# Kernel tuning notes

Hardware: AMD Instinct MI355X
Metric: run time of the kernel (lower is better)

The kernel has to match this reference:

```python
import jax, jax.numpy as jnp
import numpy as np

N_NODES = 100000
N_EDGES = 1600000
IN_CH, HID, OUT = 128, 64, 32


def gcn_conv(x, W, b, src, dst, n_nodes):
    """PyG-style GCNConv: add self-loops, sym-normalize, linear, aggregate."""
    h = x @ W  # [N, out] transform first (cheaper than transforming messages)
    loops = jnp.arange(n_nodes, dtype=src.dtype)
    s = jnp.concatenate([src, loops])
    d = jnp.concatenate([dst, loops])
    deg = jax.ops.segment_sum(jnp.ones_like(d, dtype=h.dtype), d, num_segments=n_nodes)
    dinv = jnp.where(deg > 0, jax.lax.rsqrt(deg), 0.0)
    norm = dinv[s] * dinv[d]  # [E+N]
    msg = h[s] * norm[:, None]  # gather + scale
    out = jax.ops.segment_sum(msg, d, num_segments=n_nodes)  # scatter-add
    return out + b


def setup_inputs() -> dict:
    key = jax.random.key(0)
    ks = jax.random.split(key, 8)
    x = jax.random.normal(ks[0], (N_NODES, IN_CH), dtype=jnp.float32)
    edge_index = jax.random.randint(ks[1], (2, N_EDGES), 0, N_NODES, dtype=jnp.int64)
    # Glorot-ish init for weights
    W1 = jax.random.normal(ks[2], (IN_CH, HID), dtype=jnp.float32) * (1.0 / np.sqrt(IN_CH))
    b1 = jnp.zeros((HID,), dtype=jnp.float32)
    W_mu = jax.random.normal(ks[3], (HID, OUT), dtype=jnp.float32) * (1.0 / np.sqrt(HID))
    b_mu = jnp.zeros((OUT,), dtype=jnp.float32)
    W_ls = jax.random.normal(ks[4], (HID, OUT), dtype=jnp.float32) * (1.0 / np.sqrt(HID))
    b_ls = jnp.zeros((OUT,), dtype=jnp.float32)
    return {"x": x, "edge_index": edge_index, "W1": W1, "b1": b1,
            "W_mu": W_mu, "b_mu": b_mu, "W_ls": W_ls, "b_ls": b_ls}


def reference(x, edge_index, W1, b1, W_mu, b_mu, W_ls, b_ls):
    src, dst = edge_index[0], edge_index[1]
    h = jax.nn.relu(gcn_conv(x, W1, b1, src, dst, N_NODES))
    # dropout: eval-mode identity
    mu = gcn_conv(h, W_mu, b_mu, src, dst, N_NODES)
    logstd = gcn_conv(h, W_ls, b_ls, src, dst, N_NODES)
    return (mu, logstd)
```

## Files before the change

kernel.cpp:

```cpp
#include <hip/hip_runtime.h>
#include <hip/hip_fp16.h>

#define NN 100000
#define NE 1600000
#define BKT_STRIDE 64
#define GRP 224
#define NB 447
#define SCAP 4096
#define ACHUNK 6400
#define ABLK (NE / ACHUNK)

typedef int      v2i  __attribute__((ext_vector_type(2)));
typedef int      v4i  __attribute__((ext_vector_type(4)));
typedef float    v4f  __attribute__((ext_vector_type(4)));
typedef _Float16 f16x4 __attribute__((ext_vector_type(4)));
typedef _Float16 f16x8 __attribute__((ext_vector_type(8)));
typedef float    f32x4 __attribute__((ext_vector_type(4)));

union frag_u { f16x8 v8; f16x4 v4[2]; };

__global__ __launch_bounds__(256) void k_part(const int* __restrict__ src, const int* __restrict__ dst,
                                              int* __restrict__ wc, int* __restrict__ pairs) {
  __shared__ int cntb[512];
  __shared__ int scanb[512];
  __shared__ int ofs[512];
  __shared__ int gbase[512];
  __shared__ v2i stg[ACHUNK];
  int tid = threadIdx.x;
  int e0 = blockIdx.x * ACHUNK;
  cntb[tid] = 0; cntb[tid + 256] = 0;
  __syncthreads();
  for (int k = tid; k < ACHUNK; k += 256) {
    int d = __builtin_nontemporal_load(dst + e0 + k);
    atomicAdd(&cntb[d / GRP], 1);
  }
  __syncthreads();
  scanb[tid] = cntb[tid]; scanb[tid + 256] = cntb[tid + 256];
  __syncthreads();
  for (int off = 1; off < 512; off <<= 1) {
    int a0 = (tid >= off) ? scanb[tid - off] : 0;
    int a1 = scanb[tid + 256 - off];
    __syncthreads();
    scanb[tid] += a0; scanb[tid + 256] += a1;
    __syncthreads();
  }
  ofs[tid] = scanb[tid] - cntb[tid];
  ofs[tid + 256] = scanb[tid + 256] - cntb[tid + 256];
  if (tid < NB && cntb[tid]) gbase[tid] = atomicAdd(&wc[tid], cntb[tid]);
  if (tid + 256 < NB && cntb[tid + 256]) gbase[tid + 256] = atomicAdd(&wc[tid + 256], cntb[tid + 256]);
  __syncthreads();
  for (int k = tid; k < ACHUNK; k += 256) {
    int d = __builtin_nontemporal_load(dst + e0 + k);
    int s = __builtin_nontemporal_load(src + e0 + k);
    int g = d / GRP;
    int p = atomicAdd(&ofs[g], 1);
    v2i sd; sd.x = s; sd.y = d;
    stg[p] = sd;
  }
  __syncthreads();
  for (int i = tid; i < ACHUNK; i += 256) {
    v2i sd = stg[i];
    int g = sd.y / GRP;
    int excl = scanb[g] - cntb[g];
    int o = gbase[g] + (i - excl);
    if (o < SCAP)
      pairs[(size_t)g * SCAP + o] = sd.x | ((sd.y - g * GRP) << 17);
  }
}

__global__ __launch_bounds__(256) void k_bktbuild(const int* __restrict__ pairs, const int* __restrict__ wc,
                                                  int* __restrict__ cnt, float* __restrict__ dinv,
                                                  int* __restrict__ bkt) {
  __shared__ int lb[GRP * BKT_STRIDE];
  __shared__ int lc[GRP];
  int tid = threadIdx.x;
  int g = blockIdx.x;
  int base = g * GRP;
  int nvalid = (NN - base < GRP) ? (NN - base) : GRP;
  {
    v4i sent; sent.x = NN; sent.y = NN; sent.z = NN; sent.w = NN;
    v4i* lb4 = (v4i*)lb;
#pragma unroll
    for (int i = 0; i < (GRP * BKT_STRIDE / 4) / 256; ++i) lb4[tid + 256 * i] = sent;
  }
  if (tid < GRP) lc[tid] = 0;
  __syncthreads();
  int n = wc[g];
  if (n > SCAP) n = SCAP;
  const int* seg = pairs + (size_t)g * SCAP;
  for (int i = tid; i < n; i += 256) {
    int p = seg[i];
    int s = p & 0x1FFFF;
    int dl = p >> 17;
    int pos = atomicAdd(&lc[dl], 1);
    if (pos < BKT_STRIDE) lb[dl * BKT_STRIDE + pos] = s;
  }
  __syncthreads();
  int tot4 = nvalid * BKT_STRIDE / 4;
  v4i* out4 = (v4i*)(bkt + (size_t)base * BKT_STRIDE);
  const v4i* lb4 = (const v4i*)lb;
  for (int i = tid; i < tot4; i += 256) out4[i] = lb4[i];
  if (tid < nvalid) {
    int c = lc[tid];
    if (c > BKT_STRIDE) c = BKT_STRIDE;
    cnt[base + tid] = c;
    dinv[base + tid] = rsqrtf((float)(c + 1));
  }
  if (g == 0 && tid == 0) dinv[NN] = 0.f;
}

__global__ __launch_bounds__(256) void k_gemm1(const float* __restrict__ x, const float* __restrict__ W,
                                               const float* __restrict__ dinv, __half* __restrict__ out) {
  __shared__ _Float16 Xs[64][136];
  __shared__ _Float16 Wt[64][136];
  int tid = threadIdx.x;
  int row0 = blockIdx.x * 64;
  {
    int c = tid & 63;
    int k0 = tid >> 6;
#pragma unroll
    for (int i = 0; i < 32; ++i) {
      int k = k0 + 4 * i;
      Wt[c][k] = (_Float16)W[k * 64 + c];
    }
  }
  {
#pragma unroll
    for (int i = 0; i < 8; ++i) {
      int idx = tid + 256 * i;
      int r = idx >> 5;
      int k4 = idx & 31;
      v4f v = {0.f, 0.f, 0.f, 0.f};
      if (row0 + r < NN)
        v = __builtin_nontemporal_load((const v4f*)(x + (size_t)(row0 + r) * 128 + k4 * 4));
      f16x4 h;
      h[0] = (_Float16)v.x; h[1] = (_Float16)v.y; h[2] = (_Float16)v.z; h[3] = (_Float16)v.w;
      *(f16x4*)&Xs[r][k4 * 4] = h;
    }
  }
  __syncthreads();
  int lane = tid & 63;
  int wv = tid >> 6;
  int l15 = lane & 15;
  int lq = lane >> 4;
  int rl = wv * 16 + l15;
  f32x4 acc[4] = {};
#pragma unroll
  for (int ks = 0; ks < 4; ++ks) {
    int ka = ks * 32 + lq * 4;
    frag_u bf;
    bf.v4[0] = *(const f16x4*)&Xs[rl][ka];
    bf.v4[1] = *(const f16x4*)&Xs[rl][ka + 16];
#pragma unroll
    for (int ct = 0; ct < 4; ++ct) {
      frag_u af;
      af.v4[0] = *(const f16x4*)&Wt[ct * 16 + l15][ka];
      af.v4[1] = *(const f16x4*)&Wt[ct * 16 + l15][ka + 16];
      acc[ct] = __builtin_amdgcn_mfma_f32_16x16x32_f16(af.v8, bf.v8, acc[ct], 0, 0, 0);
    }
  }
  int row = row0 + rl;
  if (row < NN) {
    float dr = dinv[row];
#pragma unroll
    for (int ct = 0; ct < 4; ++ct) {
      int c = ct * 16 + lq * 4;
      __half2 h01 = __floats2half2_rn(acc[ct][0] * dr, acc[ct][1] * dr);
      __half2 h23 = __floats2half2_rn(acc[ct][2] * dr, acc[ct][3] * dr);
      __half2* op = (__half2*)(out + (size_t)row * 64 + c);
      op[0] = h01;
      op[1] = h23;
    }
  }
}

template <bool PASS1>
__global__ __launch_bounds__(256) void k_agg(const __half* __restrict__ hin, const int* __restrict__ bkt,
                                             const int* __restrict__ cnt, const float* __restrict__ dinv,
                                             const float* __restrict__ bias, __half* __restrict__ outp) {
  int tid = threadIdx.x;
  int lane = tid & 63;
  int wv = tid >> 6;
  int node = blockIdx.x * 16 + wv * 4 + (lane >> 4);
  int ch0 = (lane & 15) * 4;
  float di = dinv[node];
  float a0, a1, a2, a3;
  {
    v2i raw = *(const v2i*)(hin + (size_t)node * 64 + ch0);
    float2 f01 = __half22float2(((const __half2*)&raw)[0]);
    float2 f23 = __half22float2(((const __half2*)&raw)[1]);
    a0 = f01.x; a1 = f01.y; a2 = f23.x; a3 = f23.y;
  }
  int n = (cnt[node] + 3) & ~3;
  const v4i* bp = (const v4i*)(bkt + node * BKT_STRIDE);
  for (int j = 0; j < n; j += 4, ++bp) {
    v4i b = *bp;
#pragma unroll
    for (int t = 0; t < 4; ++t) {
      int idx = (t == 0) ? b.x : (t == 1) ? b.y : (t == 2) ? b.z : b.w;
      v2i raw = *(const v2i*)(hin + (size_t)idx * 64 + ch0);
      float2 f01 = __half22float2(((const __half2*)&raw)[0]);
      float2 f23 = __half22float2(((const __half2*)&raw)[1]);
      a0 += f01.x; a1 += f01.y; a2 += f23.x; a3 += f23.y;
    }
  }
  float r0, r1, r2, r3;
  if (PASS1) {
    float4 bv = *(const float4*)(bias + ch0);
    r0 = di * fmaxf(di * a0 + bv.x, 0.f);
    r1 = di * fmaxf(di * a1 + bv.y, 0.f);
    r2 = di * fmaxf(di * a2 + bv.z, 0.f);
    r3 = di * fmaxf(di * a3 + bv.w, 0.f);
  } else {
    r0 = di * a0; r1 = di * a1; r2 = di * a2; r3 = di * a3;
  }
  __half2* op = (__half2*)(outp + (size_t)node * 64 + ch0);
  op[0] = __floats2half2_rn(r0, r1);
  op[1] = __floats2half2_rn(r2, r3);
}

__global__ __launch_bounds__(256) void k_gemm2(const __half* __restrict__ a, const float* __restrict__ Wmu,
                                               const float* __restrict__ Wls, const float* __restrict__ bmu,
                                               const float* __restrict__ bls, float* __restrict__ out) {
  __shared__ _Float16 Xs[64][72];
  __shared__ _Float16 Wt[64][72];
  int tid = threadIdx.x;
  int row0 = blockIdx.x * 64;
  {
    int c = tid & 63;
    int k0 = tid >> 6;
    const float* Wsrc = (c < 32) ? (Wmu + c) : (Wls + (c - 32));
#pragma unroll
    for (int i = 0; i < 16; ++i) {
      int k = k0 + 4 * i;
      Wt[c][k] = (_Float16)Wsrc[k * 32];
    }
  }
  {
#pragma unroll
    for (int i = 0; i < 2; ++i) {
      int idx = tid + 256 * i;
      int r = idx >> 3;
      int h8 = idx & 7;
      v4i raw = {0, 0, 0, 0};
      if (row0 + r < NN)
        raw = *(const v4i*)(a + (size_t)(row0 + r) * 64 + h8 * 8);
      *(v4i*)&Xs[r][h8 * 8] = raw;
    }
  }
  __syncthreads();
  int lane = tid & 63;
  int wv = tid >> 6;
  int l15 = lane & 15;
  int lq = lane >> 4;
  int rl = wv * 16 + l15;
  f32x4 acc[4] = {};
#pragma unroll
  for (int ks = 0; ks < 2; ++ks) {
    int ka = ks * 32 + lq * 4;
    frag_u bf;
    bf.v4[0] = *(const f16x4*)&Xs[rl][ka];
    bf.v4[1] = *(const f16x4*)&Xs[rl][ka + 16];
#pragma unroll
    for (int ct = 0; ct < 4; ++ct) {
      frag_u af;
      af.v4[0] = *(const f16x4*)&Wt[ct * 16 + l15][ka];
      af.v4[1] = *(const f16x4*)&Wt[ct * 16 + l15][ka + 16];
      acc[ct] = __builtin_amdgcn_mfma_f32_16x16x32_f16(af.v8, bf.v8, acc[ct], 0, 0, 0);
    }
  }
  int row = row0 + rl;
  if (row < NN) {
#pragma unroll
    for (int ct = 0; ct < 4; ++ct) {
      int c = ct * 16 + lq * 4;
      const float* bsrc = (c < 32) ? (bmu + c) : (bls + (c - 32));
      float4 o = make_float4(acc[ct][0] + bsrc[0], acc[ct][1] + bsrc[1],
                             acc[ct][2] + bsrc[2], acc[ct][3] + bsrc[3]);
      float* dst = (c < 32) ? (out + (size_t)row * 32 + c)
                            : (out + (size_t)NN * 32 + (size_t)row * 32 + (c - 32));
      *(float4*)dst = o;
    }
  }
}

extern "C" void kernel_launch(void* const* d_in, const int* in_sizes, int n_in,
                              void* d_out, int out_size, void* d_ws, size_t ws_size,
                              hipStream_t stream) {
  const float* x   = (const float*)d_in[0];
  const int*   ei  = (const int*)d_in[1];
  const float* W1  = (const float*)d_in[2];
  const float* b1  = (const float*)d_in[3];
  const float* Wmu = (const float*)d_in[4];
  const float* bmu = (const float*)d_in[5];
  const float* Wls = (const float*)d_in[6];
  const float* bls = (const float*)d_in[7];
  float* out = (float*)d_out;

  char* ws = (char*)d_ws;
  size_t off = 0;
  auto take = [&](size_t bytes) -> char* {
    char* p = ws + off;
    off = (off + bytes + 255) & ~(size_t)255;
    return p;
  };
  int*    cnt  = (int*)take((size_t)NN * 4);
  float*  dinv = (float*)take((size_t)(NN + 1) * 4);
  int*    bkt  = (int*)take((size_t)NN * BKT_STRIDE * 4);
  __half* hpre = (__half*)take((size_t)(NN + 1) * 64 * 2);
  __half* h1   = (__half*)take((size_t)(NN + 1) * 64 * 2);
  __half* agg2 = (__half*)take((size_t)(NN + 1) * 64 * 2);
  int*    wc   = (int*)take((size_t)512 * 4);

  int* pairs = (int*)hpre;

  const int* srcp = ei;
  const int* dstp = ei + NE;

  hipMemsetAsync(wc, 0, (size_t)512 * 4, stream);
  k_part<<<ABLK, 256, 0, stream>>>(srcp, dstp, wc, pairs);
  k_bktbuild<<<NB, 256, 0, stream>>>(pairs, wc, cnt, dinv, bkt);
  hipMemsetAsync(hpre + (size_t)NN * 64, 0, 64 * 2, stream);
  hipMemsetAsync(h1 + (size_t)NN * 64, 0, 64 * 2, stream);
  k_gemm1<<<(NN + 63) / 64, 256, 0, stream>>>(x, W1, dinv, hpre);
  k_agg<true><<<NN / 16, 256, 0, stream>>>(hpre, bkt, cnt, dinv, b1, h1);
  k_agg<false><<<NN / 16, 256, 0, stream>>>(h1, bkt, cnt, dinv, nullptr, agg2);
  k_gemm2<<<(NN + 63) / 64, 256, 0, stream>>>(agg2, Wmu, Wls, bmu, bls, out);
}
```

Baseline: 237.8 us.

## Fuse second aggregation into output GEMM and fold sentinel memsets into bucket build

The second neighbor aggregation now happens inside the final GEMM kernel. Each block gathers and sums rows for its 64 nodes and writes the normalized fp16 result straight into shared memory before the MFMA step. This removes the agg2 intermediate buffer's global write and read, plus one kernel launch. The two sentinel-row memsets are also folded into the bucket-build kernel. In exchange, the fused kernel runs with far fewer blocks (64 nodes per block, 4 passes per wave), which may lower memory-level parallelism for the latency-bound gathers.

```diff
diff --git a/kernel.cpp b/kernel.cpp
--- a/kernel.cpp
+++ b/kernel.cpp
@@ -70,7 +70,8 @@
 
 __global__ __launch_bounds__(256) void k_bktbuild(const int* __restrict__ pairs, const int* __restrict__ wc,
                                                   int* __restrict__ cnt, float* __restrict__ dinv,
-                                                  int* __restrict__ bkt) {
+                                                  int* __restrict__ bkt, int* __restrict__ sent0,
+                                                  int* __restrict__ sent1) {
   __shared__ int lb[GRP * BKT_STRIDE];
   __shared__ int lc[GRP];
   int tid = threadIdx.x;
@@ -84,6 +85,10 @@
     for (int i = 0; i < (GRP * BKT_STRIDE / 4) / 256; ++i) lb4[tid + 256 * i] = sent;
   }
   if (tid < GRP) lc[tid] = 0;
+  if (g == 0 && tid < 64) {
+    int* p = (tid < 32) ? sent0 : sent1;
+    p[tid & 31] = 0;
+  }
   __syncthreads();
   int n = wc[g];
   if (n > SCAP) n = SCAP;
@@ -174,10 +179,9 @@
   }
 }
 
-template <bool PASS1>
-__global__ __launch_bounds__(256) void k_agg(const __half* __restrict__ hin, const int* __restrict__ bkt,
-                                             const int* __restrict__ cnt, const float* __restrict__ dinv,
-                                             const float* __restrict__ bias, __half* __restrict__ outp) {
+__global__ __launch_bounds__(256) void k_agg1(const __half* __restrict__ hin, const int* __restrict__ bkt,
+                                              const int* __restrict__ cnt, const float* __restrict__ dinv,
+                                              const float* __restrict__ bias, __half* __restrict__ outp) {
   int tid = threadIdx.x;
   int lane = tid & 63;
   int wv = tid >> 6;
@@ -204,24 +208,21 @@
       a0 += f01.x; a1 += f01.y; a2 += f23.x; a3 += f23.y;
     }
   }
-  float r0, r1, r2, r3;
-  if (PASS1) {
-    float4 bv = *(const float4*)(bias + ch0);
-    r0 = di * fmaxf(di * a0 + bv.x, 0.f);
-    r1 = di * fmaxf(di * a1 + bv.y, 0.f);
-    r2 = di * fmaxf(di * a2 + bv.z, 0.f);
-    r3 = di * fmaxf(di * a3 + bv.w, 0.f);
-  } else {
-    r0 = di * a0; r1 = di * a1; r2 = di * a2; r3 = di * a3;
-  }
+  float4 bv = *(const float4*)(bias + ch0);
+  float r0 = di * fmaxf(di * a0 + bv.x, 0.f);
+  float r1 = di * fmaxf(di * a1 + bv.y, 0.f);
+  float r2 = di * fmaxf(di * a2 + bv.z, 0.f);
+  float r3 = di * fmaxf(di * a3 + bv.w, 0.f);
   __half2* op = (__half2*)(outp + (size_t)node * 64 + ch0);
   op[0] = __floats2half2_rn(r0, r1);
   op[1] = __floats2half2_rn(r2, r3);
 }
 
-__global__ __launch_bounds__(256) void k_gemm2(const __half* __restrict__ a, const float* __restrict__ Wmu,
-                                               const float* __restrict__ Wls, const float* __restrict__ bmu,
-                                               const float* __restrict__ bls, float* __restrict__ out) {
+__global__ __launch_bounds__(256) void k_aggemm2(const __half* __restrict__ h1, const int* __restrict__ bkt,
+                                                 const int* __restrict__ cnt, const float* __restrict__ dinv,
+                                                 const float* __restrict__ Wmu, const float* __restrict__ Wls,
+                                                 const float* __restrict__ bmu, const float* __restrict__ bls,
+                                                 float* __restrict__ out) {
   __shared__ _Float16 Xs[64][72];
   __shared__ _Float16 Wt[64][72];
   int tid = threadIdx.x;
@@ -236,21 +237,41 @@
       Wt[c][k] = (_Float16)Wsrc[k * 32];
     }
   }
-  {
-#pragma unroll
-    for (int i = 0; i < 2; ++i) {
-      int idx = tid + 256 * i;
-      int r = idx >> 3;
-      int h8 = idx & 7;
-      v4i raw = {0, 0, 0, 0};
-      if (row0 + r < NN)
-        raw = *(const v4i*)(a + (size_t)(row0 + r) * 64 + h8 * 8);
-      *(v4i*)&Xs[r][h8 * 8] = raw;
-    }
-  }
-  __syncthreads();
   int lane = tid & 63;
   int wv = tid >> 6;
+  int subn = wv * 4 + (lane >> 4);
+  int ch0 = (lane & 15) * 4;
+#pragma unroll
+  for (int it = 0; it < 4; ++it) {
+    int lr = it * 16 + subn;
+    int node = row0 + lr;
+    float a0 = 0.f, a1 = 0.f, a2 = 0.f, a3 = 0.f, di = 0.f;
+    if (node < NN) {
+      di = dinv[node];
+      v2i raw = *(const v2i*)(h1 + (size_t)node * 64 + ch0);
+      float2 f01 = __half22float2(((const __half2*)&raw)[0]);
+      float2 f23 = __half22float2(((const __half2*)&raw)[1]);
+      a0 = f01.x; a1 = f01.y; a2 = f23.x; a3 = f23.y;
+      int n = (cnt[node] + 3) & ~3;
+      const v4i* bp = (const v4i*)(bkt + node * BKT_STRIDE);
+      for (int j = 0; j < n; j += 4, ++bp) {
+        v4i b = *bp;
+#pragma unroll
+        for (int t = 0; t < 4; ++t) {
+          int idx = (t == 0) ? b.x : (t == 1) ? b.y : (t == 2) ? b.z : b.w;
+          v2i rw = *(const v2i*)(h1 + (size_t)idx * 64 + ch0);
+          float2 g01 = __half22float2(((const __half2*)&rw)[0]);
+          float2 g23 = __half22float2(((const __half2*)&rw)[1]);
+          a0 += g01.x; a1 += g01.y; a2 += g23.x; a3 += g23.y;
+        }
+      }
+    }
+    f16x4 hx;
+    hx[0] = (_Float16)(di * a0); hx[1] = (_Float16)(di * a1);
+    hx[2] = (_Float16)(di * a2); hx[3] = (_Float16)(di * a3);
+    *(f16x4*)&Xs[lr][ch0] = hx;
+  }
+  __syncthreads();
   int l15 = lane & 15;
   int lq = lane >> 4;
   int rl = wv * 16 + l15;
@@ -309,7 +330,6 @@
   int*    bkt  = (int*)take((size_t)NN * BKT_STRIDE * 4);
   __half* hpre = (__half*)take((size_t)(NN + 1) * 64 * 2);
   __half* h1   = (__half*)take((size_t)(NN + 1) * 64 * 2);
-  __half* agg2 = (__half*)take((size_t)(NN + 1) * 64 * 2);
   int*    wc   = (int*)take((size_t)512 * 4);
 
   int* pairs = (int*)hpre;
@@ -319,11 +339,9 @@
 
   hipMemsetAsync(wc, 0, (size_t)512 * 4, stream);
   k_part<<<ABLK, 256, 0, stream>>>(srcp, dstp, wc, pairs);
-  k_bktbuild<<<NB, 256, 0, stream>>>(pairs, wc, cnt, dinv, bkt);
-  hipMemsetAsync(hpre + (size_t)NN * 64, 0, 64 * 2, stream);
-  hipMemsetAsync(h1 + (size_t)NN * 64, 0, 64 * 2, stream);
+  k_bktbuild<<<NB, 256, 0, stream>>>(pairs, wc, cnt, dinv, bkt,
+                                     (int*)(hpre + (size_t)NN * 64), (int*)(h1 + (size_t)NN * 64));
   k_gemm1<<<(NN + 63) / 64, 256, 0, stream>>>(x, W1, dinv, hpre);
-  k_agg<true><<<NN / 16, 256, 0, stream>>>(hpre, bkt, cnt, dinv, b1, h1);
-  k_agg<false><<<NN / 16, 256, 0, stream>>>(h1, bkt, cnt, dinv, nullptr, agg2);
-  k_gemm2<<<(NN + 63) / 64, 256, 0, stream>>>(agg2, Wmu, Wls, bmu, bls, out);
-}
+  k_agg1<<<NN / 16, 256, 0, stream>>>(hpre, bkt, cnt, dinv, b1, h1);
+  k_aggemm2<<<(NN + 63) / 64, 256, 0, stream>>>(h1, bkt, cnt, dinv, Wmu, Wls, bmu, bls, out);
+}
```

Result: faster. 229.3 us (-3.6%).
